# Optimization experiments

Hardware: AMD Instinct MI355X
Metric: run time of the kernel (lower is better)

Reference implementation:

```python
import jax, jax.numpy as jnp
import numpy as np

N_NODES = 100000
N_PAIRS = 800000  # undirected pairs; E = 2*N_PAIRS directed edges
D_FEAT = 128
THRESHOLD = 0.01
EPS = 1e-8


def setup_inputs() -> dict:
    key = jax.random.key(0)
    k1, k2, k3, k4 = jax.random.split(key, 4)
    # symmetric edge list without self-loops (each undirected pair in both directions)
    src = jax.random.randint(k1, (N_PAIRS,), 0, N_NODES)
    off = jax.random.randint(k2, (N_PAIRS,), 1, N_NODES)
    dst = (src + off) % N_NODES  # guaranteed != src
    edge_index = jnp.stack([jnp.concatenate([src, dst]),
                            jnp.concatenate([dst, src])]).astype(jnp.int64)
    w_half = jax.random.uniform(k3, (N_PAIRS,), dtype=jnp.float32)
    edge_weight = jnp.concatenate([w_half, w_half])
    features = jax.random.normal(k4, (N_NODES, D_FEAT), dtype=jnp.float32)
    return {"edge_index": edge_index, "edge_weight": edge_weight, "features": features}


def reference(edge_index, edge_weight, features):
    # Cosine-similarity edge dropping (Jaccard.forward, non-binary feature path).
    # Original: build NxN sparse adj, take triu, per-edge cosine sim, zero edges
    # with sim < threshold, symmetrize (triu + triu^T), read back at edge positions.
    # For a symmetric duplicate-free edge list this equals per-edge masking, with
    # diagonal entries doubled by triu + triu^T.
    src, dst = edge_index[0], edge_index[1]
    node_norm = jnp.sqrt(jnp.sum(features * features, axis=-1))  # [N]
    inner = jnp.sum(features[src] * features[dst], axis=-1)       # [E] per-edge gather+dot
    sim = inner / (node_norm[src] * node_norm[dst] + EPS)
    keep = (sim >= THRESHOLD).astype(edge_weight.dtype)
    diag_double = 1.0 + (src == dst).astype(edge_weight.dtype)    # triu+triu^T doubles diagonal
    return edge_weight * keep * diag_double
```

## Files before the change

### kernel.cpp

```cpp
#include <hip/hip_runtime.h>
#include <hip/hip_fp16.h>

#define D_FEAT 128
#define THRESH 0.01f
#define EPS_F  1e-8f

typedef _Float16 half2_t __attribute__((ext_vector_type(2)));


__device__ float edge_out_scalar(const float* __restrict__ feat,
                                 float w, int s, int d) {
#pragma clang fp contract(off)
    const float* fs = feat + (size_t)s * D_FEAT;
    const float* fd = feat + (size_t)d * D_FEAT;
    float r[8], rs[8], rd[8];
#pragma unroll
    for (int j = 0; j < 8; ++j) {
        float a = fs[j], b = fd[j];
        r[j]  = a * b;
        rs[j] = a * a;
        rd[j] = b * b;
    }
    for (int k = 1; k < 16; ++k) {
#pragma unroll
        for (int j = 0; j < 8; ++j) {
            float a = fs[8 * k + j], b = fd[8 * k + j];
            r[j]  = r[j]  + a * b;
            rs[j] = rs[j] + a * a;
            rd[j] = rd[j] + b * b;
        }
    }
    float inner = ((r[0]  + r[1])  + (r[2]  + r[3]))  + ((r[4]  + r[5])  + (r[6]  + r[7]));
    float ss    = ((rs[0] + rs[1]) + (rs[2] + rs[3])) + ((rs[4] + rs[5]) + (rs[6] + rs[7]));
    float dd    = ((rd[0] + rd[1]) + (rd[2] + rd[3])) + ((rd[4] + rd[5]) + (rd[6] + rd[7]));
    float ns = __fsqrt_rn(ss);
    float nd = __fsqrt_rn(dd);
    float denom = ns * nd + EPS_F;
    float sim = inner / denom;
    float keep = (sim >= THRESH) ? 1.0f : 0.0f;
    float diag = (s == d) ? 2.0f : 1.0f;
    return (w * keep) * diag;
}

__device__ __forceinline__ float exact_sim_pairlanes(const float* __restrict__ feat,
                                                     int src, int dst, int h) {
#pragma clang fp contract(off)
    const float4* fs = (const float4*)(feat + (size_t)src * D_FEAT);
    const float4* fd = (const float4*)(feat + (size_t)dst * D_FEAT);
    float r[4], rs[4], rd[4];
    {
        float4 a = fs[h];
        float4 b = fd[h];
        r[0]  = a.x * b.x; r[1]  = a.y * b.y; r[2]  = a.z * b.z; r[3]  = a.w * b.w;
        rs[0] = a.x * a.x; rs[1] = a.y * a.y; rs[2] = a.z * a.z; rs[3] = a.w * a.w;
        rd[0] = b.x * b.x; rd[1] = b.y * b.y; rd[2] = b.z * b.z; rd[3] = b.w * b.w;
    }
#pragma unroll
    for (int k = 1; k < 16; ++k) {
        float4 a = fs[2 * k + h];
        float4 b = fd[2 * k + h];
        r[0]  = r[0]  + a.x * b.x;  r[1]  = r[1]  + a.y * b.y;
        r[2]  = r[2]  + a.z * b.z;  r[3]  = r[3]  + a.w * b.w;
        rs[0] = rs[0] + a.x * a.x;  rs[1] = rs[1] + a.y * a.y;
        rs[2] = rs[2] + a.z * a.z;  rs[3] = rs[3] + a.w * a.w;
        rd[0] = rd[0] + b.x * b.x;  rd[1] = rd[1] + b.y * b.y;
        rd[2] = rd[2] + b.z * b.z;  rd[3] = rd[3] + b.w * b.w;
    }
    float A  = (r[0]  + r[1])  + (r[2]  + r[3]);
    float As = (rs[0] + rs[1]) + (rs[2] + rs[3]);
    float Ad = (rd[0] + rd[1]) + (rd[2] + rd[3]);

    float inner = A  + __shfl_xor(A, 1, 64);
    float ssE   = As + __shfl_xor(As, 1, 64);
    float ddE   = Ad + __shfl_xor(Ad, 1, 64);

    float ns    = __fsqrt_rn(ssE);
    float nd    = __fsqrt_rn(ddE);
    float den   = ns * nd + EPS_F;
    return inner / den;
}

__device__ __forceinline__ float exact_inner_pairlanes(const float* __restrict__ feat,
                                                       int src, int dst, int h) {
#pragma clang fp contract(off)
    const float4* fs = (const float4*)(feat + (size_t)src * D_FEAT);
    const float4* fd = (const float4*)(feat + (size_t)dst * D_FEAT);
    float r[4];
    {
        float4 a = fs[h];
        float4 b = fd[h];
        r[0] = a.x * b.x; r[1] = a.y * b.y; r[2] = a.z * b.z; r[3] = a.w * b.w;
    }
#pragma unroll
    for (int k = 1; k < 16; ++k) {
        float4 a = fs[2 * k + h];
        float4 b = fd[2 * k + h];
        r[0] = r[0] + a.x * b.x;  r[1] = r[1] + a.y * b.y;
        r[2] = r[2] + a.z * b.z;  r[3] = r[3] + a.w * b.w;
    }
    float A = (r[0] + r[1]) + (r[2] + r[3]);
    return A + __shfl_xor(A, 1, 64);
}

__global__ __launch_bounds__(256) void jaccard_edge_kernel(
    const int* __restrict__ ei, const float* __restrict__ w,
    const float* __restrict__ feat, float* __restrict__ out,
    int P, int E)
{
    int t    = blockIdx.x * blockDim.x + threadIdx.x;
    int pair = t >> 1;
    int half = t & 1;
    if (pair >= P) return;

    int src = ei[pair];
    int dst = ei[E + pair];

    float sim  = exact_sim_pairlanes(feat, src, dst, half);
    float keep = (sim >= THRESH) ? 1.0f : 0.0f;

    if (half == 0) {
        float diag = (src == dst) ? 2.0f : 1.0f;
        out[pair] = (w[pair] * keep) * diag;
        int m = P + pair;
        if (m < E) {
            int s2 = ei[m];
            int d2 = ei[E + m];
            if (s2 == dst && d2 == src) out[m] = (w[m] * keep) * diag;
            else                        out[m] = edge_out_scalar(feat, w[m], s2, d2);
        }
    }
}

__global__ __launch_bounds__(256) void norm_convert_kernel(
    const float* __restrict__ feat, __half* __restrict__ hfeat,
    float* __restrict__ nrm, int nNodes)
{
#pragma clang fp contract(off)
    int t = blockIdx.x * blockDim.x + threadIdx.x;
    int node = t >> 1;
    int h    = t & 1;
    if (node >= nNodes) return;

    const float4* fs  = (const float4*)(feat + (size_t)node * D_FEAT);
    uint2*        hro = (uint2*)(hfeat + (size_t)node * D_FEAT);

    float rs[4];
    {
        float4 a = fs[h];
        rs[0] = a.x * a.x; rs[1] = a.y * a.y; rs[2] = a.z * a.z; rs[3] = a.w * a.w;
        __half2 h0 = __floats2half2_rn(a.x, a.y);
        __half2 h1 = __floats2half2_rn(a.z, a.w);
        uint2 o;
        o.x = __builtin_bit_cast(unsigned int, h0);
        o.y = __builtin_bit_cast(unsigned int, h1);
        hro[h] = o;
    }
#pragma unroll
    for (int k = 1; k < 16; ++k) {
        float4 a = fs[2 * k + h];
        rs[0] = rs[0] + a.x * a.x;  rs[1] = rs[1] + a.y * a.y;
        rs[2] = rs[2] + a.z * a.z;  rs[3] = rs[3] + a.w * a.w;
        __half2 h0 = __floats2half2_rn(a.x, a.y);
        __half2 h1 = __floats2half2_rn(a.z, a.w);
        uint2 o;
        o.x = __builtin_bit_cast(unsigned int, h0);
        o.y = __builtin_bit_cast(unsigned int, h1);
        hro[2 * k + h] = o;
    }
    float As = (rs[0] + rs[1]) + (rs[2] + rs[3]);
    float ss = As + __shfl_xor(As, 1, 64);
    if (h == 0) nrm[node] = __fsqrt_rn(ss);
}

__device__ __forceinline__ float dot8_f16(uint4 ua, uint4 ub, float acc) {
    acc = __builtin_amdgcn_fdot2(__builtin_bit_cast(half2_t, ua.x),
                                 __builtin_bit_cast(half2_t, ub.x), acc, false);
    acc = __builtin_amdgcn_fdot2(__builtin_bit_cast(half2_t, ua.y),
                                 __builtin_bit_cast(half2_t, ub.y), acc, false);
    acc = __builtin_amdgcn_fdot2(__builtin_bit_cast(half2_t, ua.z),
                                 __builtin_bit_cast(half2_t, ub.z), acc, false);
    acc = __builtin_amdgcn_fdot2(__builtin_bit_cast(half2_t, ua.w),
                                 __builtin_bit_cast(half2_t, ub.w), acc, false);
    return acc;
}

__global__ __launch_bounds__(256) void jaccard_edge_f16n_kernel(
    const int* __restrict__ ei, const float* __restrict__ w,
    const float* __restrict__ feat, const __half* __restrict__ hfeat,
    const float* __restrict__ nrm, float* __restrict__ out, int P, int E)
{
#pragma clang fp contract(off)
    int t    = blockIdx.x * blockDim.x + threadIdx.x;
    int pair = t >> 1;
    int h    = t & 1;
    if (pair >= P) return;

    int src = ei[pair];
    int dst = ei[E + pair];

    const uint4* ha = (const uint4*)(hfeat + (size_t)src * D_FEAT);
    const uint4* hb = (const uint4*)(hfeat + (size_t)dst * D_FEAT);

    uint4 A[8], B[8];
#pragma unroll
    for (int k = 0; k < 8; ++k) {
        A[k] = ha[2 * k + h];
        B[k] = hb[2 * k + h];
    }
    float na = nrm[src];
    float nb = nrm[dst];

    float d = 0.f;
#pragma unroll
    for (int k = 0; k < 8; ++k) d = dot8_f16(A[k], B[k], d);

    float dot = d + __shfl_xor(d, 1, 64);

    float prod = na * nb;
    float den  = prod + EPS_F;
    float sim  = dot / den;

    float bnd  = (1.1e-3f * prod + 4e-7f * (na + nb)) / den + 1e-6f;
    float diff = sim - THRESH;

    float keep;
    if (fabsf(diff) > bnd) {
        keep = (diff >= 0.f) ? 1.0f : 0.0f;
    } else {
        float inner = exact_inner_pairlanes(feat, src, dst, h);
        float se    = inner / den;
        keep = (se >= THRESH) ? 1.0f : 0.0f;
    }

    if (h == 0) {
        float diag = (src == dst) ? 2.0f : 1.0f;
        out[pair] = (w[pair] * keep) * diag;
        int m = P + pair;
        if (m < E) {
            int s2 = ei[m];
            int d2 = ei[E + m];
            if (s2 == dst && d2 == src) out[m] = (w[m] * keep) * diag;
            else                        out[m] = edge_out_scalar(feat, w[m], s2, d2);
        }
    }
}

extern "C" void kernel_launch(void* const* d_in, const int* in_sizes, int n_in,
                              void* d_out, int out_size, void* d_ws, size_t ws_size,
                              hipStream_t stream) {
    const int*   ei   = (const int*)d_in[0];
    const float* w    = (const float*)d_in[1];
    const float* feat = (const float*)d_in[2];
    float*       out  = (float*)d_out;

    int E = in_sizes[1];
    int P = E - E / 2;
    long nfeat = in_sizes[2];
    long nNodes = nfeat / D_FEAT;
    size_t need = (size_t)nfeat * sizeof(__half) + (size_t)nNodes * sizeof(float);

    if (ws_size < need || (nfeat % D_FEAT) != 0) {
        int threads = 2 * P;
        int grid = (threads + 255) / 256;
        jaccard_edge_kernel<<<grid, 256, 0, stream>>>(ei, w, feat, out, P, E);
        return;
    }

    __half* hfeat = (__half*)d_ws;
    float*  nrm   = (float*)((char*)d_ws + (size_t)nfeat * sizeof(__half));

    int tA = 2 * (int)nNodes;
    norm_convert_kernel<<<(tA + 255) / 256, 256, 0, stream>>>(feat, hfeat, nrm, (int)nNodes);

    int tB = 2 * P;
    jaccard_edge_f16n_kernel<<<(tB + 255) / 256, 256, 0, stream>>>(
        ei, w, feat, hfeat, nrm, out, P, E);
}
```

Measured before the change: 171.2 us.

## Prenormalize fp16 features, split each pair over four lanes, skip norm loads

The norm/convert pass now scales each row by its inverse norm before fp16 conversion, so the edge kernel's dot product is the cosine directly. Rows with tiny or non-finite norms are marked with NaN sentinels that force the exact fallback. The edge kernel drops the per-edge norm gathers and the division, spreads each pair over four lanes instead of two, and uses nontemporal loads and stores for streaming index and output traffic. This trades extra register pressure in the conversion kernel and a fixed error bound for fewer per-edge loads and more memory-level parallelism in the gather.

```diff
diff --git a/kernel.cpp b/kernel.cpp
--- a/kernel.cpp
+++ b/kernel.cpp
@@ -144,32 +144,43 @@
     const float4* fs  = (const float4*)(feat + (size_t)node * D_FEAT);
     uint2*        hro = (uint2*)(hfeat + (size_t)node * D_FEAT);
 
+    float4 row[16];
     float rs[4];
     {
         float4 a = fs[h];
+        row[0] = a;
         rs[0] = a.x * a.x; rs[1] = a.y * a.y; rs[2] = a.z * a.z; rs[3] = a.w * a.w;
-        __half2 h0 = __floats2half2_rn(a.x, a.y);
-        __half2 h1 = __floats2half2_rn(a.z, a.w);
-        uint2 o;
-        o.x = __builtin_bit_cast(unsigned int, h0);
-        o.y = __builtin_bit_cast(unsigned int, h1);
-        hro[h] = o;
     }
 #pragma unroll
     for (int k = 1; k < 16; ++k) {
         float4 a = fs[2 * k + h];
+        row[k] = a;
         rs[0] = rs[0] + a.x * a.x;  rs[1] = rs[1] + a.y * a.y;
         rs[2] = rs[2] + a.z * a.z;  rs[3] = rs[3] + a.w * a.w;
-        __half2 h0 = __floats2half2_rn(a.x, a.y);
-        __half2 h1 = __floats2half2_rn(a.z, a.w);
-        uint2 o;
-        o.x = __builtin_bit_cast(unsigned int, h0);
-        o.y = __builtin_bit_cast(unsigned int, h1);
-        hro[2 * k + h] = o;
     }
     float As = (rs[0] + rs[1]) + (rs[2] + rs[3]);
     float ss = As + __shfl_xor(As, 1, 64);
-    if (h == 0) nrm[node] = __fsqrt_rn(ss);
+    float na = __fsqrt_rn(ss);
+    if (h == 0) nrm[node] = na;
+
+    bool ok = isfinite(na) && (na >= 0.03f);
+    float r = 1.0f / na;
+
+#pragma unroll
+    for (int k = 0; k < 16; ++k) {
+        uint2 o;
+        if (ok) {
+            float4 a = row[k];
+            __half2 h0 = __floats2half2_rn(a.x * r, a.y * r);
+            __half2 h1 = __floats2half2_rn(a.z * r, a.w * r);
+            o.x = __builtin_bit_cast(unsigned int, h0);
+            o.y = __builtin_bit_cast(unsigned int, h1);
+        } else {
+            o.x = 0x7FFF7FFFu;
+            o.y = 0x7FFF7FFFu;
+        }
+        hro[2 * k + h] = o;
+    }
 }
 
 __device__ __forceinline__ float dot8_f16(uint4 ua, uint4 ub, float acc) {
@@ -184,63 +195,65 @@
     return acc;
 }
 
-__global__ __launch_bounds__(256) void jaccard_edge_f16n_kernel(
+__global__ __launch_bounds__(256) void jaccard_edge_f16u_kernel(
     const int* __restrict__ ei, const float* __restrict__ w,
     const float* __restrict__ feat, const __half* __restrict__ hfeat,
     const float* __restrict__ nrm, float* __restrict__ out, int P, int E)
 {
 #pragma clang fp contract(off)
     int t    = blockIdx.x * blockDim.x + threadIdx.x;
-    int pair = t >> 1;
-    int h    = t & 1;
+    int pair = t >> 2;
+    int q    = t & 3;
     if (pair >= P) return;
 
-    int src = ei[pair];
-    int dst = ei[E + pair];
+    int src = __builtin_nontemporal_load(ei + pair);
+    int dst = __builtin_nontemporal_load(ei + E + pair);
 
     const uint4* ha = (const uint4*)(hfeat + (size_t)src * D_FEAT);
     const uint4* hb = (const uint4*)(hfeat + (size_t)dst * D_FEAT);
 
-    uint4 A[8], B[8];
-#pragma unroll
-    for (int k = 0; k < 8; ++k) {
-        A[k] = ha[2 * k + h];
-        B[k] = hb[2 * k + h];
-    }
-    float na = nrm[src];
-    float nb = nrm[dst];
+    uint4 A[4], B[4];
+#pragma unroll
+    for (int k = 0; k < 4; ++k) {
+        A[k] = ha[4 * k + q];
+        B[k] = hb[4 * k + q];
+    }
 
     float d = 0.f;
 #pragma unroll
-    for (int k = 0; k < 8; ++k) d = dot8_f16(A[k], B[k], d);
-
-    float dot = d + __shfl_xor(d, 1, 64);
-
-    float prod = na * nb;
-    float den  = prod + EPS_F;
-    float sim  = dot / den;
-
-    float bnd  = (1.1e-3f * prod + 4e-7f * (na + nb)) / den + 1e-6f;
-    float diff = sim - THRESH;
+    for (int k = 0; k < 4; ++k) d = dot8_f16(A[k], B[k], d);
+
+    d += __shfl_xor(d, 1, 64);
+    float dot = d + __shfl_xor(d, 2, 64);
+
+    float diff = dot - THRESH;
+    const float bnd = 1.2e-3f;
 
     float keep;
-    if (fabsf(diff) > bnd) {
+    if (fabsf(diff) > bnd && fabsf(dot) < 2.0f) {
         keep = (diff >= 0.f) ? 1.0f : 0.0f;
     } else {
-        float inner = exact_inner_pairlanes(feat, src, dst, h);
-        float se    = inner / den;
+        float se = 0.f;
+        if (q < 2) {
+            float inner = exact_inner_pairlanes(feat, src, dst, q);
+            float den   = nrm[src] * nrm[dst] + EPS_F;
+            se = inner / den;
+        }
         keep = (se >= THRESH) ? 1.0f : 0.0f;
     }
 
-    if (h == 0) {
+    if (q == 0) {
         float diag = (src == dst) ? 2.0f : 1.0f;
-        out[pair] = (w[pair] * keep) * diag;
+        __builtin_nontemporal_store((w[pair] * keep) * diag, out + pair);
         int m = P + pair;
         if (m < E) {
-            int s2 = ei[m];
-            int d2 = ei[E + m];
-            if (s2 == dst && d2 == src) out[m] = (w[m] * keep) * diag;
-            else                        out[m] = edge_out_scalar(feat, w[m], s2, d2);
+            int s2 = __builtin_nontemporal_load(ei + m);
+            int d2 = __builtin_nontemporal_load(ei + E + m);
+            if (s2 == dst && d2 == src) {
+                __builtin_nontemporal_store((w[m] * keep) * diag, out + m);
+            } else {
+                out[m] = edge_out_scalar(feat, w[m], s2, d2);
+            }
         }
     }
 }
@@ -272,7 +285,7 @@
     int tA = 2 * (int)nNodes;
     norm_convert_kernel<<<(tA + 255) / 256, 256, 0, stream>>>(feat, hfeat, nrm, (int)nNodes);
 
-    int tB = 2 * P;
-    jaccard_edge_f16n_kernel<<<(tB + 255) / 256, 256, 0, stream>>>(
+    int tB = 4 * P;
+    jaccard_edge_f16u_kernel<<<(tB + 255) / 256, 256, 0, stream>>>(
         ei, w, feat, hfeat, nrm, out, P, E);
 }
```

Measured after the change: 157.6 us. 1.09x faster.
